# Optimization experiments

Hardware: AMD Instinct MI355X
Metric: run time of the kernel (lower is better)

The kernel has to match this reference:

```python
import jax, jax.numpy as jnp
import numpy as np

B, IN, H = 4096, 1024, 1024


def setup_inputs() -> dict:
    key = jax.random.key(0)
    ks = jax.random.split(key, 16)
    u = lambda k, shape: jax.random.uniform(k, shape, jnp.float32, -0.1, 0.1)
    return {
        "x": jax.random.normal(ks[0], (B, IN), jnp.float32),
        "h_prev": jax.random.normal(ks[1], (B, H), jnp.float32),
        "c_prev": jax.random.normal(ks[2], (B, H), jnp.float32),
        "W_ii": u(ks[3], (H, IN)), "W_hi": u(ks[4], (H, H)), "b_i": u(ks[5], (H,)),
        "W_if": u(ks[6], (H, IN)), "W_hf": u(ks[7], (H, H)), "b_f": u(ks[8], (H,)),
        "W_ig": u(ks[9], (H, IN)), "W_hg": u(ks[10], (H, H)), "b_g": u(ks[11], (H,)),
        "W_io": u(ks[12], (H, IN)), "W_ho": u(ks[13], (H, H)), "b_o": u(ks[14], (H,)),
    }


def reference(x, h_prev, c_prev, W_ii, W_hi, b_i, W_if, W_hf, b_f,
              W_ig, W_hg, b_g, W_io, W_ho, b_o):
    # Fuse the 8 gate GEMMs into 2 concatenated-weight GEMMs: [B,IN]@[IN,4H] and [B,H]@[H,4H]
    W_x = jnp.concatenate([W_ii, W_if, W_ig, W_io], axis=0)  # [4H, IN]
    W_h = jnp.concatenate([W_hi, W_hf, W_hg, W_ho], axis=0)  # [4H, H]
    b = jnp.concatenate([b_i, b_f, b_g, b_o])                # [4H]
    gates = x @ W_x.T + h_prev @ W_h.T + b                   # [B, 4H]
    i_t, f_t, g_t, o_t = jnp.split(gates, 4, axis=-1)
    i_t = jax.nn.sigmoid(i_t)
    f_t = jax.nn.sigmoid(f_t)
    g_t = jnp.tanh(g_t)
    o_t = jax.nn.sigmoid(o_t)
    c_t = f_t * c_prev + i_t * g_t
    h_t = o_t * jnp.tanh(c_t)
    return (h_t, (h_t, c_t))
```

## Files before the change

kernel.cpp:

```cpp
#include <hip/hip_runtime.h>
#include <hip/hip_bf16.h>
#include <stdint.h>

#define B_DIM 4096
#define IN_DIM 1024
#define H_DIM 1024
#define K_DIM 2048
#define BH (B_DIM * H_DIM)
#define NT 32

typedef __bf16 bf16x8 __attribute__((ext_vector_type(8)));
typedef float  f32x4  __attribute__((ext_vector_type(4)));

__device__ __forceinline__ unsigned short f2b(float f) {
  uint32_t u = __builtin_bit_cast(uint32_t, f);
  u += 0x7fffu + ((u >> 16) & 1u);
  return (unsigned short)(u >> 16);
}

__device__ __forceinline__ void load_lds16(const void* g, void* l) {
  __builtin_amdgcn_global_load_lds(
      (const __attribute__((address_space(1))) uint32_t*)g,
      (__attribute__((address_space(3))) uint32_t*)l, 16, 0, 0);
}

__device__ __forceinline__ void bar() {
  asm volatile("" ::: "memory");
  __builtin_amdgcn_s_barrier();
  asm volatile("" ::: "memory");
}

__device__ __forceinline__ float sigmoidf_(float x) {
  return 1.0f / (1.0f + __expf(-x));
}
__device__ __forceinline__ float tanhf_(float x) {
  float e = __expf(-2.0f * x);
  return (1.0f - e) / (1.0f + e);
}

__global__ void pack_all(const float* __restrict__ x, const float* __restrict__ h,
                         const float* __restrict__ Wii, const float* __restrict__ Wif,
                         const float* __restrict__ Wig, const float* __restrict__ Wio,
                         const float* __restrict__ Whi, const float* __restrict__ Whf,
                         const float* __restrict__ Whg, const float* __restrict__ Who,
                         unsigned short* __restrict__ A, unsigned short* __restrict__ Wp) {
  const int bid = blockIdx.x;
  if (bid < 8192) {
    int t = bid * 256 + threadIdx.x;
    int e = t * 4;
    int b = e >> 11;
    int k = e & 2047;
    const float* src = (k < IN_DIM) ? (x + (size_t)b * IN_DIM + k)
                                    : (h + (size_t)b * H_DIM + (k - IN_DIM));
    f32x4 v = *(const f32x4*)src;
    ushort4 o;
    o.x = f2b(v[0]); o.y = f2b(v[1]); o.z = f2b(v[2]); o.w = f2b(v[3]);
    *(ushort4*)(A + (size_t)b * K_DIM + k) = o;
  } else {
    int t = (bid - 8192) * 256 + threadIdx.x;
    int e = t * 4;
    int n = e >> 11;
    int k = e & 2047;
    int r = n & 255;
    int gate = ((r >> 7) << 1) | ((r >> 4) & 1);
    int j = ((n >> 8) << 6) + (((r >> 5) & 3) << 4) + (r & 15);
    const float* Wx = (gate == 0) ? Wii : (gate == 1) ? Wif : (gate == 2) ? Wig : Wio;
    const float* Wh = (gate == 0) ? Whi : (gate == 1) ? Whf : (gate == 2) ? Whg : Who;
    const float* src = (k < IN_DIM) ? (Wx + (size_t)j * IN_DIM + k)
                                    : (Wh + (size_t)j * H_DIM + (k - IN_DIM));
    f32x4 v = *(const f32x4*)src;
    ushort4 o;
    o.x = f2b(v[0]); o.y = f2b(v[1]); o.z = f2b(v[2]); o.w = f2b(v[3]);
    *(ushort4*)(Wp + (size_t)n * K_DIM + k) = o;
  }
}


#define VM8 asm volatile("s_waitcnt vmcnt(8)" ::: "memory")
#define VM4 asm volatile("s_waitcnt vmcnt(4)" ::: "memory")
#define VM2 asm volatile("s_waitcnt vmcnt(2)" ::: "memory")
#define VM0 asm volatile("s_waitcnt vmcnt(0)" ::: "memory")

#define STAGE(ldsbase, gbase, kelem) do {                                        \
  const unsigned short* g0_ = (gbase) + (size_t)srow0 * K_DIM + (kelem) + schunk * 8; \
  load_lds16(g0_, (ldsbase) + tid * 8);                                          \
  load_lds16(g0_ + (size_t)64 * K_DIM, (ldsbase) + 4096 + tid * 8);              \
} while (0)

#define PHASE(SLOT, MQ, NQ, STAGE_STMT, VM_WAIT) do {                            \
  const unsigned short* As_ = &lds[SLOT][0][MQ][0];                              \
  const unsigned short* Bs_ = &lds[SLOT][1][NQ][0];                              \
  bf16x8 af[4][2], bq[2][2];                                                     \
  _Pragma("unroll")                                                              \
  for (int m = 0; m < 4; ++m) {                                                  \
    int ro = (wr * 64 + m * 16 + lrow) * 64;                                     \
    af[m][0] = *(const bf16x8*)(As_ + ro + ks0);                                 \
    af[m][1] = *(const bf16x8*)(As_ + ro + ks1);                                 \
  }                                                                              \
  _Pragma("unroll")                                                              \
  for (int n = 0; n < 2; ++n) {                                                  \
    int ro = (wc * 32 + n * 16 + lrow) * 64;                                     \
    bq[n][0] = *(const bf16x8*)(Bs_ + ro + ks0);                                 \
    bq[n][1] = *(const bf16x8*)(Bs_ + ro + ks1);                                 \
  }                                                                              \
  STAGE_STMT;                                                                    \
  bar();                                                                         \
  asm volatile("s_waitcnt lgkmcnt(0)" ::: "memory");                             \
  __builtin_amdgcn_sched_barrier(0);                                             \
  __builtin_amdgcn_s_setprio(1);                                                 \
  _Pragma("unroll")                                                              \
  for (int m = 0; m < 4; ++m)                                                    \
    _Pragma("unroll")                                                            \
    for (int n = 0; n < 2; ++n) {                                                \
      acc[MQ][NQ][m][n] = __builtin_amdgcn_mfma_f32_16x16x32_bf16(               \
          af[m][0], bq[n][0], acc[MQ][NQ][m][n], 0, 0, 0);                       \
      acc[MQ][NQ][m][n] = __builtin_amdgcn_mfma_f32_16x16x32_bf16(               \
          af[m][1], bq[n][1], acc[MQ][NQ][m][n], 0, 0, 0);                       \
    }                                                                            \
  __builtin_amdgcn_s_setprio(0);                                                 \
  __builtin_amdgcn_sched_barrier(0);                                             \
  VM_WAIT;                                                                       \
  bar();                                                                         \
} while (0)

__global__ __launch_bounds__(512, 2) void gemm_lstm(
    const unsigned short* __restrict__ A,
    const unsigned short* __restrict__ Wp,
    const float* __restrict__ c_prev,
    const float* __restrict__ b_i, const float* __restrict__ b_f,
    const float* __restrict__ b_g, const float* __restrict__ b_o,
    float* __restrict__ out) {
  __shared__ unsigned short lds[2][2][2][128 * 64];

  const int tid  = threadIdx.x;
  const int lane = tid & 63;
  const int wid  = tid >> 6;
  const int wr   = wid >> 2;
  const int wc   = wid & 3;
  const int lrow = lane & 15;

  const int b0 = blockIdx.x;
  const int w  = (b0 & 7) * 32 + (b0 >> 3);
  const int bx = w & 15;
  const int by = w >> 4;

  const unsigned short* Ag = A  + (size_t)by * 256 * K_DIM;
  const unsigned short* Wg = Wp + (size_t)bx * 256 * K_DIM;

  const int srow0  = tid >> 3;
  const int schunk = (tid & 7) ^ (srow0 & 7);
  const int ks0 = ((lane >> 4) * 8) ^ ((lane & 7) << 3);
  const int ks1 = ks0 ^ 32;

  f32x4 acc[2][2][4][2];
#pragma unroll
  for (int a = 0; a < 2; ++a)
#pragma unroll
    for (int b = 0; b < 2; ++b)
#pragma unroll
      for (int m = 0; m < 4; ++m)
#pragma unroll
        for (int n = 0; n < 2; ++n) acc[a][b][m][n] = (f32x4){0.f, 0.f, 0.f, 0.f};

  STAGE(&lds[0][0][0][0], Ag, 0);
  STAGE(&lds[0][1][0][0], Wg, 0);
  STAGE(&lds[0][0][1][0], Ag + 128 * K_DIM, 0);
  STAGE(&lds[0][1][1][0], Wg + 128 * K_DIM, 0);
  STAGE(&lds[1][0][0][0], Ag, 64);
  STAGE(&lds[1][1][0][0], Wg, 64);
  VM4;
  bar();

  for (int t2 = 0; t2 < NT - 2; t2 += 2) {
    {
      const int k1 = (t2 + 1) * 64, k2 = (t2 + 2) * 64;
      PHASE(0, 0, 0, STAGE(&lds[1][1][1][0], Wg + 128 * K_DIM, k1), VM8);
      PHASE(0, 0, 1, STAGE(&lds[1][0][1][0], Ag + 128 * K_DIM, k1), VM8);
      PHASE(0, 1, 0, STAGE(&lds[0][0][0][0], Ag, k2), );
      PHASE(0, 1, 1, STAGE(&lds[0][1][0][0], Wg, k2), VM8);
    }
    {
      const int k1 = (t2 + 2) * 64, k2 = (t2 + 3) * 64;
      PHASE(1, 0, 0, STAGE(&lds[0][1][1][0], Wg + 128 * K_DIM, k1), VM8);
      PHASE(1, 0, 1, STAGE(&lds[0][0][1][0], Ag + 128 * K_DIM, k1), VM8);
      PHASE(1, 1, 0, STAGE(&lds[1][0][0][0], Ag, k2), );
      PHASE(1, 1, 1, STAGE(&lds[1][1][0][0], Wg, k2), VM8);
    }
  }
  {
    const int k1 = (NT - 1) * 64;
    PHASE(0, 0, 0, STAGE(&lds[1][1][1][0], Wg + 128 * K_DIM, k1), VM8);
    PHASE(0, 0, 1, STAGE(&lds[1][0][1][0], Ag + 128 * K_DIM, k1), VM8);
    PHASE(0, 1, 0, , );
    PHASE(0, 1, 1, , VM4);
    PHASE(1, 0, 0, , VM2);
    PHASE(1, 0, 1, , VM0);
    PHASE(1, 1, 0, , );
    PHASE(1, 1, 1, , );
  }

  const int j  = bx * 64 + wc * 16 + lrow;
  const float biv = b_i[j], bfv = b_f[j], bgv = b_g[j], bov = b_o[j];
  const int rb = by * 256 + wr * 64 + (lane >> 4) * 4;
#pragma unroll
  for (int mq = 0; mq < 2; ++mq)
#pragma unroll
    for (int m = 0; m < 4; ++m)
#pragma unroll
      for (int r = 0; r < 4; ++r) {
        const int row = rb + mq * 128 + m * 16 + r;
        const float iv = sigmoidf_(acc[mq][0][m][0][r] + biv);
        const float fv = sigmoidf_(acc[mq][0][m][1][r] + bfv);
        const float gv = tanhf_(acc[mq][1][m][0][r] + bgv);
        const float ov = sigmoidf_(acc[mq][1][m][1][r] + bov);
        const size_t idx = (size_t)row * H_DIM + j;
        const float cv = fv * c_prev[idx] + iv * gv;
        const float hv = ov * tanhf_(cv);
        out[idx]          = hv;
        out[BH + idx]     = hv;
        out[2 * BH + idx] = cv;
      }
}

extern "C" void kernel_launch(void* const* d_in, const int* in_sizes, int n_in,
                              void* d_out, int out_size, void* d_ws, size_t ws_size,
                              hipStream_t stream) {
  const float* x   = (const float*)d_in[0];
  const float* hp  = (const float*)d_in[1];
  const float* cp  = (const float*)d_in[2];
  const float* Wii = (const float*)d_in[3];
  const float* Whi = (const float*)d_in[4];
  const float* bi  = (const float*)d_in[5];
  const float* Wif = (const float*)d_in[6];
  const float* Whf = (const float*)d_in[7];
  const float* bf  = (const float*)d_in[8];
  const float* Wig = (const float*)d_in[9];
  const float* Whg = (const float*)d_in[10];
  const float* bg  = (const float*)d_in[11];
  const float* Wio = (const float*)d_in[12];
  const float* Who = (const float*)d_in[13];
  const float* bo  = (const float*)d_in[14];

  unsigned short* Abf = (unsigned short*)d_ws;
  unsigned short* Wbf = (unsigned short*)((char*)d_ws + (16u << 20));
  float*          out = (float*)d_out;

  pack_all<<<16384, 256, 0, stream>>>(x, hp, Wii, Wif, Wig, Wio,
                                      Whi, Whf, Whg, Who, Abf, Wbf);
  gemm_lstm<<<256, 512, 0, stream>>>(Abf, Wbf, cp, bi, bf, bg, bo, out);
}
```

Measured before the change: 214.9 us.

## Reorder quadrant MFMA phases to reuse LDS fragments and deepen prefetch

Restructures the per-tile phase schedule so the quadrant order (0,0),(0,1),(1,1),(1,0) reuses A or B register fragments between consecutive phases. B fragments for both N-quadrants are held in registers, which cuts redundant LDS reads. The staging order and vmcnt waits are reworked to issue global-to-LDS loads further ahead, with the next tile's first B fragment read at the end of each tile. This adds register pressure under the 512x2 launch bounds and makes the wait counts harder to get right.

After: 210.6 us. 2.0% less time.

```diff
diff --git a/kernel.cpp b/kernel.cpp
--- a/kernel.cpp
+++ b/kernel.cpp
@@ -76,9 +76,7 @@
 }
 
 
-#define VM8 asm volatile("s_waitcnt vmcnt(8)" ::: "memory")
-#define VM4 asm volatile("s_waitcnt vmcnt(4)" ::: "memory")
-#define VM2 asm volatile("s_waitcnt vmcnt(2)" ::: "memory")
+#define VM6 asm volatile("s_waitcnt vmcnt(6)" ::: "memory")
 #define VM0 asm volatile("s_waitcnt vmcnt(0)" ::: "memory")
 
 #define STAGE(ldsbase, gbase, kelem) do {                                        \
@@ -87,40 +85,49 @@
   load_lds16(g0_ + (size_t)64 * K_DIM, (ldsbase) + 4096 + tid * 8);              \
 } while (0)
 
-#define PHASE(SLOT, MQ, NQ, STAGE_STMT, VM_WAIT) do {                            \
-  const unsigned short* As_ = &lds[SLOT][0][MQ][0];                              \
-  const unsigned short* Bs_ = &lds[SLOT][1][NQ][0];                              \
-  bf16x8 af[4][2], bq[2][2];                                                     \
+#define RA(S, MQ) do {                                                           \
   _Pragma("unroll")                                                              \
   for (int m = 0; m < 4; ++m) {                                                  \
-    int ro = (wr * 64 + m * 16 + lrow) * 64;                                     \
-    af[m][0] = *(const bf16x8*)(As_ + ro + ks0);                                 \
-    af[m][1] = *(const bf16x8*)(As_ + ro + ks1);                                 \
+    const unsigned short* p_ = &lds[S][0][MQ][(wr * 64 + m * 16 + lrow) * 64];   \
+    af[m][0] = *(const bf16x8*)(p_ + ks0);                                       \
+    af[m][1] = *(const bf16x8*)(p_ + ks1);                                       \
   }                                                                              \
+} while (0)
+
+#define RB(S, NQ) do {                                                           \
   _Pragma("unroll")                                                              \
   for (int n = 0; n < 2; ++n) {                                                  \
-    int ro = (wc * 32 + n * 16 + lrow) * 64;                                     \
-    bq[n][0] = *(const bf16x8*)(Bs_ + ro + ks0);                                 \
-    bq[n][1] = *(const bf16x8*)(Bs_ + ro + ks1);                                 \
+    const unsigned short* p_ = &lds[S][1][NQ][(wc * 32 + n * 16 + lrow) * 64];   \
+    bq[NQ][n][0] = *(const bf16x8*)(p_ + ks0);                                   \
+    bq[NQ][n][1] = *(const bf16x8*)(p_ + ks1);                                   \
   }                                                                              \
-  STAGE_STMT;                                                                    \
-  bar();                                                                         \
+} while (0)
+
+#define SYNC do { bar();                                                         \
   asm volatile("s_waitcnt lgkmcnt(0)" ::: "memory");                             \
-  __builtin_amdgcn_sched_barrier(0);                                             \
+  __builtin_amdgcn_sched_barrier(0); } while (0)
+
+#define EPH do { __builtin_amdgcn_sched_barrier(0); bar(); } while (0)
+
+#define MM(MQ, NQ) do {                                                          \
   __builtin_amdgcn_s_setprio(1);                                                 \
   _Pragma("unroll")                                                              \
   for (int m = 0; m < 4; ++m)                                                    \
     _Pragma("unroll")                                                            \
     for (int n = 0; n < 2; ++n) {                                                \
       acc[MQ][NQ][m][n] = __builtin_amdgcn_mfma_f32_16x16x32_bf16(               \
-          af[m][0], bq[n][0], acc[MQ][NQ][m][n], 0, 0, 0);                       \
+          af[m][0], bq[NQ][n][0], acc[MQ][NQ][m][n], 0, 0, 0);                   \
       acc[MQ][NQ][m][n] = __builtin_amdgcn_mfma_f32_16x16x32_bf16(               \
-          af[m][1], bq[n][1], acc[MQ][NQ][m][n], 0, 0, 0);                       \
+          af[m][1], bq[NQ][n][1], acc[MQ][NQ][m][n], 0, 0, 0);                   \
     }                                                                            \
   __builtin_amdgcn_s_setprio(0);                                                 \
-  __builtin_amdgcn_sched_barrier(0);                                             \
-  VM_WAIT;                                                                       \
-  bar();                                                                         \
+} while (0)
+
+#define TILE(S, STG1, STG2, STG3, STG4, VMW, NEXTB) do {                         \
+  RA(S, 0); STG1; SYNC; MM(0, 0); EPH;                                           \
+  RB(S, 1); STG2; SYNC; MM(0, 1); EPH;                                           \
+  RA(S, 1); STG3; SYNC; MM(1, 1); EPH;                                           \
+  STG4;     SYNC; MM(1, 0); VMW; NEXTB; EPH;                                     \
 } while (0)
 
 __global__ __launch_bounds__(512, 2) void gemm_lstm(
@@ -152,6 +159,9 @@
   const int ks0 = ((lane >> 4) * 8) ^ ((lane & 7) << 3);
   const int ks1 = ks0 ^ 32;
 
+  bf16x8 af[4][2];
+  bf16x8 bq[2][2][2];
+
   f32x4 acc[2][2][4][2];
 #pragma unroll
   for (int a = 0; a < 2; ++a)
@@ -164,40 +174,34 @@
 
   STAGE(&lds[0][0][0][0], Ag, 0);
   STAGE(&lds[0][1][0][0], Wg, 0);
+  STAGE(&lds[0][1][1][0], Wg + 128 * K_DIM, 0);
   STAGE(&lds[0][0][1][0], Ag + 128 * K_DIM, 0);
-  STAGE(&lds[0][1][1][0], Wg + 128 * K_DIM, 0);
   STAGE(&lds[1][0][0][0], Ag, 64);
-  STAGE(&lds[1][1][0][0], Wg, 64);
-  VM4;
+  STAGE(&lds[1][1][1][0], Wg + 128 * K_DIM, 64);
+  STAGE(&lds[1][0][1][0], Ag + 128 * K_DIM, 64);
+  VM6;
   bar();
-
-  for (int t2 = 0; t2 < NT - 2; t2 += 2) {
-    {
-      const int k1 = (t2 + 1) * 64, k2 = (t2 + 2) * 64;
-      PHASE(0, 0, 0, STAGE(&lds[1][1][1][0], Wg + 128 * K_DIM, k1), VM8);
-      PHASE(0, 0, 1, STAGE(&lds[1][0][1][0], Ag + 128 * K_DIM, k1), VM8);
-      PHASE(0, 1, 0, STAGE(&lds[0][0][0][0], Ag, k2), );
-      PHASE(0, 1, 1, STAGE(&lds[0][1][0][0], Wg, k2), VM8);
-    }
-    {
-      const int k1 = (t2 + 2) * 64, k2 = (t2 + 3) * 64;
-      PHASE(1, 0, 0, STAGE(&lds[0][1][1][0], Wg + 128 * K_DIM, k1), VM8);
-      PHASE(1, 0, 1, STAGE(&lds[0][0][1][0], Ag + 128 * K_DIM, k1), VM8);
-      PHASE(1, 1, 0, STAGE(&lds[1][0][0][0], Ag, k2), );
-      PHASE(1, 1, 1, STAGE(&lds[1][1][0][0], Wg, k2), VM8);
-    }
+  RB(0, 0);
+
+  for (int t2 = 0; t2 < 30; t2 += 2) {
+    const int kA = (t2 + 1) * 64;
+    const int kB = (t2 + 2) * 64;
+    const int kC = (t2 + 3) * 64;
+    TILE(0,
+         STAGE(&lds[1][1][0][0], Wg, kA),
+         STAGE(&lds[0][0][0][0], Ag, kB),
+         STAGE(&lds[0][1][1][0], Wg + 128 * K_DIM, kB),
+         STAGE(&lds[0][0][1][0], Ag + 128 * K_DIM, kB),
+         VM6, RB(1, 0));
+    TILE(1,
+         STAGE(&lds[0][1][0][0], Wg, kB),
+         STAGE(&lds[1][0][0][0], Ag, kC),
+         STAGE(&lds[1][1][1][0], Wg + 128 * K_DIM, kC),
+         STAGE(&lds[1][0][1][0], Ag + 128 * K_DIM, kC),
+         VM6, RB(0, 0));
   }
-  {
-    const int k1 = (NT - 1) * 64;
-    PHASE(0, 0, 0, STAGE(&lds[1][1][1][0], Wg + 128 * K_DIM, k1), VM8);
-    PHASE(0, 0, 1, STAGE(&lds[1][0][1][0], Ag + 128 * K_DIM, k1), VM8);
-    PHASE(0, 1, 0, , );
-    PHASE(0, 1, 1, , VM4);
-    PHASE(1, 0, 0, , VM2);
-    PHASE(1, 0, 1, , VM0);
-    PHASE(1, 1, 0, , );
-    PHASE(1, 1, 1, , );
-  }
+  TILE(0, STAGE(&lds[1][1][0][0], Wg, 31 * 64), , , , VM0, RB(1, 0));
+  TILE(1, , , , , , );
 
   const int j  = bx * 64 + wc * 16 + lrow;
   const float biv = b_i[j], bfv = b_f[j], bgv = b_g[j], bov = b_o[j];
```
